# Kernel tuning notes

Hardware: AMD Instinct MI355X
Metric: run time of the kernel (lower is better)

Reference implementation:

```python
import jax, jax.numpy as jnp
import numpy as np

N = 50000
E = 640000
IN_DIM = 128
HIDDEN = 128
OUT_DIM = 128


def setup_inputs() -> dict:
    key = jax.random.key(0)
    ks = jax.random.split(key, 8)
    x = jax.random.normal(ks[0], (N, IN_DIM), dtype=jnp.float32)
    edge_index = jax.random.randint(ks[1], (2, E), 0, N, dtype=jnp.int64)
    s = 1.0 / np.sqrt(IN_DIM)
    w1l = jax.random.uniform(ks[2], (HIDDEN, IN_DIM), minval=-s, maxval=s, dtype=jnp.float32)
    b1 = jax.random.uniform(ks[3], (HIDDEN,), minval=-s, maxval=s, dtype=jnp.float32)
    w1r = jax.random.uniform(ks[4], (HIDDEN, IN_DIM), minval=-s, maxval=s, dtype=jnp.float32)
    s2 = 1.0 / np.sqrt(HIDDEN)
    w2l = jax.random.uniform(ks[5], (OUT_DIM, HIDDEN), minval=-s2, maxval=s2, dtype=jnp.float32)
    b2 = jax.random.uniform(ks[6], (OUT_DIM,), minval=-s2, maxval=s2, dtype=jnp.float32)
    w2r = jax.random.uniform(ks[7], (OUT_DIM, HIDDEN), minval=-s2, maxval=s2, dtype=jnp.float32)
    return {"x": x, "edge_index": edge_index, "w1l": w1l, "b1": b1, "w1r": w1r,
            "w2l": w2l, "b2": b2, "w2r": w2r}


def sage_conv(x, src, dst, wl, bl, wr):
    # mean-aggregate source features at destination nodes
    msg = x[src]                                   # [E, d]
    agg = jax.ops.segment_sum(msg, dst, num_segments=N)   # [N, d]
    cnt = jax.ops.segment_sum(jnp.ones((src.shape[0],), x.dtype), dst, num_segments=N)
    agg = agg / jnp.maximum(cnt, 1.0)[:, None]
    # PyG SAGEConv: lin_l(agg) + lin_r(x); bias lives in lin_l
    return agg @ wl.T + bl + x @ wr.T


def reference(x, edge_index, w1l, b1, w1r, w2l, b2, w2r):
    src, dst = edge_index[0], edge_index[1]
    h = jax.nn.relu(sage_conv(x, src, dst, w1l, b1, w1r))
    out = sage_conv(h, src, dst, w2l, b2, w2r)
    return out
```

## Files before the change

### kernel.cpp

```cpp
#include <hip/hip_runtime.h>

#define DIM 128
#define CAP 64
#define FSTRIDE 16
#define PBLK 640

typedef _Float16 half8 __attribute__((ext_vector_type(8)));
typedef float floatx4 __attribute__((ext_vector_type(4)));
typedef unsigned short ushort8 __attribute__((ext_vector_type(8)));

__global__ void k_setup(const floatx4* __restrict__ in4, half8* __restrict__ out8,
                        const float* __restrict__ w1l, const float* __restrict__ w1r,
                        half8* __restrict__ Wf1,
                        const float* __restrict__ w2l, const float* __restrict__ w2r,
                        half8* __restrict__ Wf2,
                        const int* __restrict__ src, const int* __restrict__ dst,
                        int* __restrict__ fillS, unsigned short* __restrict__ pad,
                        int n8, int N, int E){
  int b = blockIdx.x;
  if (b < 8*PBLK){
    const int p = b & 7, c = b >> 3;
    const int PN = (N + 7) >> 3;
    const int n0 = p * PN;
    const int n1 = (n0 + PN < N) ? n0 + PN : N;
    const int CE = (E + PBLK - 1) / PBLK;
    const int e0 = c * CE;
    const int e1 = (e0 + CE < E) ? e0 + CE : E;
    if ((e0 & 3) == 0){
      const int nvec = (e1 - e0) & ~3;
      for (int eb = e0 + threadIdx.x*4; eb < e0 + nvec; eb += 1024){
        int4 d4 = *(const int4*)(dst + eb);
        int4 s4 = *(const int4*)(src + eb);
        #pragma unroll
        for (int u = 0; u < 4; ++u){
          int d = (&d4.x)[u];
          if (d >= n0 && d < n1){
            int q = atomicAdd(&fillS[d*FSTRIDE], 1);
            if (q < CAP) pad[d*CAP + q] = (unsigned short)((&s4.x)[u]);
          }
        }
      }
      for (int e = e0 + nvec + threadIdx.x; e < e1; e += 256){
        int d = dst[e];
        if (d >= n0 && d < n1){
          int s = src[e];
          int q = atomicAdd(&fillS[d*FSTRIDE], 1);
          if (q < CAP) pad[d*CAP + q] = (unsigned short)s;
        }
      }
    } else {
      for (int e = e0 + threadIdx.x; e < e1; e += 256){
        int d = dst[e];
        if (d >= n0 && d < n1){
          int s = src[e];
          int q = atomicAdd(&fillS[d*FSTRIDE], 1);
          if (q < CAP) pad[d*CAP + q] = (unsigned short)s;
        }
      }
    }
  } else if (b < 8*PBLK + ((n8 + 255) >> 8)){
    int i = (b - 8*PBLK)*256 + threadIdx.x;
    if (i < n8){
      floatx4 a = in4[2*i], c = in4[2*i + 1];
      half8 h;
      h[0] = (_Float16)a[0]; h[1] = (_Float16)a[1];
      h[2] = (_Float16)a[2]; h[3] = (_Float16)a[3];
      h[4] = (_Float16)c[0]; h[5] = (_Float16)c[1];
      h[6] = (_Float16)c[2]; h[7] = (_Float16)c[3];
      out8[i] = h;
    }
  } else {
    int which = b - 8*PBLK - ((n8 + 255) >> 8);
    const float* wl = (which < 16) ? w1l : w2l;
    const float* wr = (which < 16) ? w1r : w2r;
    half8* Wf = (which < 16) ? Wf1 : Wf2;
    int t = (which & 15)*256 + threadIdx.x;
    int ks = t >> 9, jt = (t >> 6) & 7, lane = t & 63;
    int j = jt*16 + (lane & 15);
    int kb = ks*32 + (lane >> 4)*8;
    half8 h;
    #pragma unroll
    for (int i = 0; i < 8; ++i){
      int k = kb + i;
      float v = (k < 128) ? wl[j*128 + k] : wr[j*128 + (k - 128)];
      h[i] = (_Float16)v;
    }
    Wf[t] = h;
  }
}

template<bool RELU, bool OUT_HALF>
__global__ __launch_bounds__(256) void k_fused(
    const half8* __restrict__ featH8, const unsigned short* __restrict__ pad,
    const int* __restrict__ fillS, const half8* __restrict__ Wf,
    const float* __restrict__ bias, void* __restrict__ outp, int n)
{
  __shared__ _Float16 aggL[16][136];
  const int tid = threadIdx.x;
  const int node0 = blockIdx.x * 16;

  {
    const int ch = tid & 15;
    const int ml = tid >> 4;
    const int node = node0 + ml;
    float acc[8] = {0,0,0,0,0,0,0,0};
    float sc = 0.0f;
    if (node < n){
      int deg = fillS[node*FSTRIDE];
      int cnt = (deg < CAP) ? deg : CAP;
      const int base = node*CAP;
      for (int p = 0; p < cnt; p += 8){
        ushort8 si = *(const ushort8*)&pad[base + p];
        int   s[8];
        float w[8];
        #pragma unroll
        for (int u = 0; u < 8; ++u){
          bool valid = (p + u) < cnt;
          s[u] = valid ? (int)si[u] : 0;
          w[u] = valid ? 1.0f : 0.0f;
        }
        half8 v[8];
        #pragma unroll
        for (int u = 0; u < 8; ++u) v[u] = featH8[s[u]*16 + ch];
        #pragma unroll
        for (int u = 0; u < 8; ++u){
          #pragma unroll
          for (int i = 0; i < 8; ++i) acc[i] += w[u] * (float)v[u][i];
        }
      }
      sc = 1.0f / fmaxf((float)deg, 1.0f);
    }
    half8 o;
    #pragma unroll
    for (int i = 0; i < 8; ++i) o[i] = (_Float16)(acc[i]*sc);
    *(half8*)&aggL[ml][ch*8] = o;
  }
  __syncthreads();

  const int lane = tid & 63, wv = tid >> 6;
  const int m = lane & 15, quad = lane >> 4;
  const int arow = node0 + m;
  const int rowSafe = (arow < n) ? arow : 0;

  floatx4 acc2[2] = {{0,0,0,0},{0,0,0,0}};

  #pragma unroll
  for (int ks = 0; ks < 8; ++ks){
    half8 a;
    if (ks < 4){
      a = *(const half8*)&aggL[m][(ks*4 + quad)*8];
    } else {
      a = featH8[rowSafe*16 + (ks-4)*4 + quad];
      if (arow >= n) a = half8{};
    }
    #pragma unroll
    for (int jl = 0; jl < 2; ++jl){
      int jt = wv*2 + jl;
      half8 bb = Wf[(ks*8 + jt)*64 + lane];
      acc2[jl] = __builtin_amdgcn_mfma_f32_16x16x32_f16(a, bb, acc2[jl], 0, 0, 0);
    }
  }

  #pragma unroll
  for (int jl = 0; jl < 2; ++jl){
    int j = (wv*2 + jl)*16 + m;
    float bj = bias[j];
    #pragma unroll
    for (int r = 0; r < 4; ++r){
      int node = node0 + quad*4 + r;
      if (node < n){
        float v = acc2[jl][r] + bj;
        if (RELU) v = fmaxf(v, 0.f);
        if (OUT_HALF) ((_Float16*)outp)[node*DIM + j] = (_Float16)v;
        else          ((float*)outp)[node*DIM + j] = v;
      }
    }
  }
}

extern "C" void kernel_launch(void* const* d_in, const int* in_sizes, int n_in,
                              void* d_out, int out_size, void* d_ws, size_t ws_size,
                              hipStream_t stream)
{
  const float* x   = (const float*)d_in[0];
  const int*   ei  = (const int*)d_in[1];
  const float* w1l = (const float*)d_in[2];
  const float* b1  = (const float*)d_in[3];
  const float* w1r = (const float*)d_in[4];
  const float* w2l = (const float*)d_in[5];
  const float* b2  = (const float*)d_in[6];
  const float* w2r = (const float*)d_in[7];
  float* out = (float*)d_out;

  const int N = in_sizes[0] / DIM;
  const int E = in_sizes[1] / 2;

  char* p = (char*)d_ws;
  auto carve = [&](size_t bytes) -> char* {
    char* q = p;
    p += (bytes + 255) & ~(size_t)255;
    return q;
  };
  _Float16*       xh    = (_Float16*)carve((size_t)N * DIM * 2);
  _Float16*       hh    = (_Float16*)carve((size_t)N * DIM * 2);
  half8*          Wf1   = (half8*)carve(4096 * 16);
  half8*          Wf2   = (half8*)carve(4096 * 16);
  int*            fillS = (int*)carve((size_t)N * FSTRIDE * 4);
  unsigned short* pad   = (unsigned short*)carve((size_t)N * CAP * 2);

  const int* src = ei;
  const int* dst = ei + E;

  const int n8 = N * DIM / 8;
  const int bCast = (n8 + 255)/256;

  hipMemsetAsync(fillS, 0, (size_t)N * FSTRIDE * 4, stream);

  k_setup<<<8*PBLK + bCast + 32, 256, 0, stream>>>(
      (const floatx4*)x, (half8*)xh, w1l, w1r, Wf1, w2l, w2r, Wf2,
      src, dst, fillS, pad, n8, N, E);

  const int gF = (N + 15)/16;

  k_fused<true, true><<<gF, 256, 0, stream>>>(
      (const half8*)xh, pad, fillS, Wf1, b1, (void*)hh, N);
  k_fused<false, false><<<gF, 256, 0, stream>>>(
      (const half8*)hh, pad, fillS, Wf2, b2, (void*)out, N);
}
```

Baseline: 199.3 us.

## Fuse setup, scatter and both SAGE layers into one cooperative persistent kernel

Replaces the memset, the setup kernel and the two layer kernels with a single cooperatively launched kernel. A grid-wide sync separates the phases: zeroing plus fp16 casting plus weight packing, then CSR-like scatter, then layer 1, then layer 2. Each block loops over node tiles persistently. This removes several kernel launches and the separate memset. In exchange it adds grid-barrier cost and less parallelism in the scatter phase, and it keeps the old multi-kernel path as a fallback.

```diff
diff --git a/kernel.cpp b/kernel.cpp
--- a/kernel.cpp
+++ b/kernel.cpp
@@ -1,103 +1,27 @@
 #include <hip/hip_runtime.h>
+#include <hip/hip_cooperative_groups.h>
+
+namespace cg = cooperative_groups;
 
 #define DIM 128
 #define CAP 64
 #define FSTRIDE 16
+#define GRID_MEGA 1563
 #define PBLK 640
 
 typedef _Float16 half8 __attribute__((ext_vector_type(8)));
 typedef float floatx4 __attribute__((ext_vector_type(4)));
 typedef unsigned short ushort8 __attribute__((ext_vector_type(8)));
 
-__global__ void k_setup(const floatx4* __restrict__ in4, half8* __restrict__ out8,
-                        const float* __restrict__ w1l, const float* __restrict__ w1r,
-                        half8* __restrict__ Wf1,
-                        const float* __restrict__ w2l, const float* __restrict__ w2r,
-                        half8* __restrict__ Wf2,
-                        const int* __restrict__ src, const int* __restrict__ dst,
-                        int* __restrict__ fillS, unsigned short* __restrict__ pad,
-                        int n8, int N, int E){
-  int b = blockIdx.x;
-  if (b < 8*PBLK){
-    const int p = b & 7, c = b >> 3;
-    const int PN = (N + 7) >> 3;
-    const int n0 = p * PN;
-    const int n1 = (n0 + PN < N) ? n0 + PN : N;
-    const int CE = (E + PBLK - 1) / PBLK;
-    const int e0 = c * CE;
-    const int e1 = (e0 + CE < E) ? e0 + CE : E;
-    if ((e0 & 3) == 0){
-      const int nvec = (e1 - e0) & ~3;
-      for (int eb = e0 + threadIdx.x*4; eb < e0 + nvec; eb += 1024){
-        int4 d4 = *(const int4*)(dst + eb);
-        int4 s4 = *(const int4*)(src + eb);
-        #pragma unroll
-        for (int u = 0; u < 4; ++u){
-          int d = (&d4.x)[u];
-          if (d >= n0 && d < n1){
-            int q = atomicAdd(&fillS[d*FSTRIDE], 1);
-            if (q < CAP) pad[d*CAP + q] = (unsigned short)((&s4.x)[u]);
-          }
-        }
-      }
-      for (int e = e0 + nvec + threadIdx.x; e < e1; e += 256){
-        int d = dst[e];
-        if (d >= n0 && d < n1){
-          int s = src[e];
-          int q = atomicAdd(&fillS[d*FSTRIDE], 1);
-          if (q < CAP) pad[d*CAP + q] = (unsigned short)s;
-        }
-      }
-    } else {
-      for (int e = e0 + threadIdx.x; e < e1; e += 256){
-        int d = dst[e];
-        if (d >= n0 && d < n1){
-          int s = src[e];
-          int q = atomicAdd(&fillS[d*FSTRIDE], 1);
-          if (q < CAP) pad[d*CAP + q] = (unsigned short)s;
-        }
-      }
-    }
-  } else if (b < 8*PBLK + ((n8 + 255) >> 8)){
-    int i = (b - 8*PBLK)*256 + threadIdx.x;
-    if (i < n8){
-      floatx4 a = in4[2*i], c = in4[2*i + 1];
-      half8 h;
-      h[0] = (_Float16)a[0]; h[1] = (_Float16)a[1];
-      h[2] = (_Float16)a[2]; h[3] = (_Float16)a[3];
-      h[4] = (_Float16)c[0]; h[5] = (_Float16)c[1];
-      h[6] = (_Float16)c[2]; h[7] = (_Float16)c[3];
-      out8[i] = h;
-    }
-  } else {
-    int which = b - 8*PBLK - ((n8 + 255) >> 8);
-    const float* wl = (which < 16) ? w1l : w2l;
-    const float* wr = (which < 16) ? w1r : w2r;
-    half8* Wf = (which < 16) ? Wf1 : Wf2;
-    int t = (which & 15)*256 + threadIdx.x;
-    int ks = t >> 9, jt = (t >> 6) & 7, lane = t & 63;
-    int j = jt*16 + (lane & 15);
-    int kb = ks*32 + (lane >> 4)*8;
-    half8 h;
-    #pragma unroll
-    for (int i = 0; i < 8; ++i){
-      int k = kb + i;
-      float v = (k < 128) ? wl[j*128 + k] : wr[j*128 + (k - 128)];
-      h[i] = (_Float16)v;
-    }
-    Wf[t] = h;
-  }
-}
-
 template<bool RELU, bool OUT_HALF>
-__global__ __launch_bounds__(256) void k_fused(
+__device__ __forceinline__ void fused_tile(
     const half8* __restrict__ featH8, const unsigned short* __restrict__ pad,
     const int* __restrict__ fillS, const half8* __restrict__ Wf,
-    const float* __restrict__ bias, void* __restrict__ outp, int n)
-{
-  __shared__ _Float16 aggL[16][136];
+    const float* __restrict__ bias, void* __restrict__ outp, int n,
+    int tile, _Float16 (&aggL)[16][136])
+{
   const int tid = threadIdx.x;
-  const int node0 = blockIdx.x * 16;
+  const int node0 = tile * 16;
 
   {
     const int ch = tid & 15;
@@ -178,6 +102,151 @@
   }
 }
 
+__device__ __forceinline__ void prep_weights(int which, const float* __restrict__ w1l,
+    const float* __restrict__ w1r, half8* __restrict__ Wf1,
+    const float* __restrict__ w2l, const float* __restrict__ w2r,
+    half8* __restrict__ Wf2)
+{
+  const float* wl = (which < 16) ? w1l : w2l;
+  const float* wr = (which < 16) ? w1r : w2r;
+  half8* Wf = (which < 16) ? Wf1 : Wf2;
+  int t = (which & 15)*256 + threadIdx.x;
+  int ks = t >> 9, jt = (t >> 6) & 7, lane = t & 63;
+  int j = jt*16 + (lane & 15);
+  int kb = ks*32 + (lane >> 4)*8;
+  half8 h;
+  #pragma unroll
+  for (int i = 0; i < 8; ++i){
+    int k = kb + i;
+    float v = (k < 128) ? wl[j*128 + k] : wr[j*128 + (k - 128)];
+    h[i] = (_Float16)v;
+  }
+  Wf[t] = h;
+}
+
+__global__ void __launch_bounds__(256, 7) k_mega(
+    const floatx4* __restrict__ in4, _Float16* __restrict__ xh, _Float16* __restrict__ hh,
+    const float* __restrict__ w1l, const float* __restrict__ b1, const float* __restrict__ w1r,
+    const float* __restrict__ w2l, const float* __restrict__ b2, const float* __restrict__ w2r,
+    half8* __restrict__ Wf1, half8* __restrict__ Wf2,
+    const int* __restrict__ src, const int* __restrict__ dst,
+    int* __restrict__ fillS, unsigned short* __restrict__ pad,
+    float* __restrict__ out, int N, int E)
+{
+  __shared__ _Float16 aggL[16][136];
+  cg::grid_group grid = cg::this_grid();
+  const int b = blockIdx.x, tid = threadIdx.x;
+  const int gsz = gridDim.x;
+
+  {
+    int4* f4 = (int4*)fillS;
+    const int nf4 = N * FSTRIDE / 4;
+    for (int i = b*256 + tid; i < nf4; i += gsz*256) f4[i] = int4{0,0,0,0};
+    const int n8 = N * (DIM/8);
+    half8* out8 = (half8*)xh;
+    for (int i = b*256 + tid; i < n8; i += gsz*256){
+      floatx4 a = in4[2*i], c = in4[2*i + 1];
+      half8 h;
+      h[0] = (_Float16)a[0]; h[1] = (_Float16)a[1];
+      h[2] = (_Float16)a[2]; h[3] = (_Float16)a[3];
+      h[4] = (_Float16)c[0]; h[5] = (_Float16)c[1];
+      h[6] = (_Float16)c[2]; h[7] = (_Float16)c[3];
+      out8[i] = h;
+    }
+    if (b >= 32 && b < 64)
+      prep_weights(b - 32, w1l, w1r, Wf1, w2l, w2r, Wf2);
+  }
+  grid.sync();
+
+  {
+    const int p = b & 7, c = b >> 3;
+    const int nc = (gsz - p + 7) >> 3;
+    const int PN = (N + 7) >> 3;
+    const int n0 = p * PN;
+    const int n1 = (n0 + PN < N) ? n0 + PN : N;
+    const int CE = ((E + nc - 1) / nc + 3) & ~3;
+    const int e0 = c * CE;
+    const int e1 = (e0 + CE < E) ? e0 + CE : E;
+    for (int eb = e0 + tid*4; eb < e1; eb += 1024){
+      int4 d4 = *(const int4*)(dst + eb);
+      int4 s4 = *(const int4*)(src + eb);
+      #pragma unroll
+      for (int u = 0; u < 4; ++u){
+        int d = (&d4.x)[u];
+        if (d >= n0 && d < n1){
+          int q = atomicAdd(&fillS[d*FSTRIDE], 1);
+          if (q < CAP) pad[d*CAP + q] = (unsigned short)((&s4.x)[u]);
+        }
+      }
+    }
+  }
+  grid.sync();
+
+  const int nTiles = (N + 15) >> 4;
+  for (int t = b; t < nTiles; t += gsz){
+    fused_tile<true, true>((const half8*)xh, pad, fillS, Wf1, b1, (void*)hh, N, t, aggL);
+    __syncthreads();
+  }
+  grid.sync();
+
+  for (int t = b; t < nTiles; t += gsz){
+    fused_tile<false, false>((const half8*)hh, pad, fillS, Wf2, b2, (void*)out, N, t, aggL);
+    __syncthreads();
+  }
+}
+
+__global__ void k_setup(const floatx4* __restrict__ in4, half8* __restrict__ out8,
+                        const float* __restrict__ w1l, const float* __restrict__ w1r,
+                        half8* __restrict__ Wf1,
+                        const float* __restrict__ w2l, const float* __restrict__ w2r,
+                        half8* __restrict__ Wf2,
+                        const int* __restrict__ src, const int* __restrict__ dst,
+                        int* __restrict__ fillS, unsigned short* __restrict__ pad,
+                        int n8, int N, int E){
+  int b = blockIdx.x;
+  if (b < 8*PBLK){
+    const int p = b & 7, c = b >> 3;
+    const int PN = (N + 7) >> 3;
+    const int n0 = p * PN;
+    const int n1 = (n0 + PN < N) ? n0 + PN : N;
+    const int CE = (E + PBLK - 1) / PBLK;
+    const int e0 = c * CE;
+    const int e1 = (e0 + CE < E) ? e0 + CE : E;
+    for (int e = e0 + threadIdx.x; e < e1; e += 256){
+      int d = dst[e];
+      if (d >= n0 && d < n1){
+        int s = src[e];
+        int q = atomicAdd(&fillS[d*FSTRIDE], 1);
+        if (q < CAP) pad[d*CAP + q] = (unsigned short)s;
+      }
+    }
+  } else if (b < 8*PBLK + ((n8 + 255) >> 8)){
+    int i = (b - 8*PBLK)*256 + threadIdx.x;
+    if (i < n8){
+      floatx4 a = in4[2*i], c = in4[2*i + 1];
+      half8 h;
+      h[0] = (_Float16)a[0]; h[1] = (_Float16)a[1];
+      h[2] = (_Float16)a[2]; h[3] = (_Float16)a[3];
+      h[4] = (_Float16)c[0]; h[5] = (_Float16)c[1];
+      h[6] = (_Float16)c[2]; h[7] = (_Float16)c[3];
+      out8[i] = h;
+    }
+  } else {
+    int which = b - 8*PBLK - ((n8 + 255) >> 8);
+    prep_weights(which, w1l, w1r, Wf1, w2l, w2r, Wf2);
+  }
+}
+
+template<bool RELU, bool OUT_HALF>
+__global__ __launch_bounds__(256) void k_fused(
+    const half8* __restrict__ featH8, const unsigned short* __restrict__ pad,
+    const int* __restrict__ fillS, const half8* __restrict__ Wf,
+    const float* __restrict__ bias, void* __restrict__ outp, int n)
+{
+  __shared__ _Float16 aggL[16][136];
+  fused_tile<RELU, OUT_HALF>(featH8, pad, fillS, Wf, bias, outp, n, blockIdx.x, aggL);
+}
+
 extern "C" void kernel_launch(void* const* d_in, const int* in_sizes, int n_in,
                               void* d_out, int out_size, void* d_ws, size_t ws_size,
                               hipStream_t stream)
@@ -211,19 +280,37 @@
   const int* src = ei;
   const int* dst = ei + E;
 
-  const int n8 = N * DIM / 8;
-  const int bCast = (n8 + 255)/256;
-
-  hipMemsetAsync(fillS, 0, (size_t)N * FSTRIDE * 4, stream);
-
-  k_setup<<<8*PBLK + bCast + 32, 256, 0, stream>>>(
-      (const floatx4*)x, (half8*)xh, w1l, w1r, Wf1, w2l, w2r, Wf2,
-      src, dst, fillS, pad, n8, N, E);
-
-  const int gF = (N + 15)/16;
-
-  k_fused<true, true><<<gF, 256, 0, stream>>>(
-      (const half8*)xh, pad, fillS, Wf1, b1, (void*)hh, N);
-  k_fused<false, false><<<gF, 256, 0, stream>>>(
-      (const half8*)hh, pad, fillS, Wf2, b2, (void*)out, N);
-}
+  static int coopOK = -1;
+  if (coopOK < 0){
+    int bpc = 0;
+    hipError_t err = hipOccupancyMaxActiveBlocksPerMultiprocessor(&bpc, k_mega, 256, 0);
+    coopOK = (err == hipSuccess && bpc * 256 >= GRID_MEGA) ? 1 : 0;
+  }
+
+  if (coopOK){
+    const floatx4* in4 = (const floatx4*)x;
+    int Nv = N, Ev = E;
+    void* args[] = {
+      (void*)&in4, (void*)&xh, (void*)&hh,
+      (void*)&w1l, (void*)&b1, (void*)&w1r,
+      (void*)&w2l, (void*)&b2, (void*)&w2r,
+      (void*)&Wf1, (void*)&Wf2,
+      (void*)&src, (void*)&dst,
+      (void*)&fillS, (void*)&pad,
+      (void*)&out, (void*)&Nv, (void*)&Ev
+    };
+    hipLaunchCooperativeKernel(k_mega, dim3(GRID_MEGA), dim3(256), args, 0, stream);
+  } else {
+    const int n8 = N * DIM / 8;
+    const int bCast = (n8 + 255)/256;
+    hipMemsetAsync(fillS, 0, (size_t)N * FSTRIDE * 4, stream);
+    k_setup<<<8*PBLK + bCast + 32, 256, 0, stream>>>(
+        (const floatx4*)x, (half8*)xh, w1l, w1r, Wf1, w2l, w2r, Wf2,
+        src, dst, fillS, pad, n8, N, E);
+    const int gF = (N + 15)/16;
+    k_fused<true, true><<<gF, 256, 0, stream>>>(
+        (const half8*)xh, pad, fillS, Wf1, b1, (void*)hh, N);
+    k_fused<false, false><<<gF, 256, 0, stream>>>(
+        (const half8*)hh, pad, fillS, Wf2, b2, (void*)out, N);
+  }
+}
```

After: 199.8 us. No clear change (+0.3%).
